# Optimization experiments

Hardware: AMD Instinct MI355X
Metric: run time of the kernel (lower is better)

The kernel has to match this reference:

```python
import jax, jax.numpy as jnp
import numpy as np

D = 512
H = 8
HD = D // H
EPS = 1e-5
NEG_INF = -1e30


def _ln(x, g, b):
    mu = jnp.mean(x, axis=-1, keepdims=True)
    var = jnp.mean(jnp.square(x - mu), axis=-1, keepdims=True)
    return (x - mu) * jax.lax.rsqrt(var + EPS) * g + b


def setup_inputs() -> dict:
    key = jax.random.key(0)
    ks = jax.random.split(key, 8)
    V, M, S = 128, 128, 514  # seq includes 2 head tokens (cls+dist)
    inp = {
        "video_embeds": jax.random.normal(ks[0], (V, D), jnp.float32),
        "music_features": jax.random.normal(ks[1], (M, S, D), jnp.float32),
        "music_masks": jnp.ones((M, S - 2), jnp.int32),
    }
    wk = jax.random.split(ks[2], 5)
    for name, k in zip(["Wq", "Wk", "Wv", "Wo", "Wl"], wk):
        inp[name] = jax.random.normal(k, (D, D), jnp.float32) * 0.02
    for name in ["bq", "bk", "bv", "bo", "bl"]:
        inp[name] = jnp.zeros((D,), jnp.float32)
    for name in ["g1", "g2", "g3"]:
        inp[name] = jnp.ones((D,), jnp.float32)
    for name in ["b1", "b2", "b3"]:
        inp[name] = jnp.zeros((D,), jnp.float32)
    return inp


def reference(video_embeds, music_features, music_masks,
              Wq, bq, Wk, bk, Wv, bv, Wo, bo, Wl, bl,
              g1, b1, g2, b2, g3, b3):
    # drop cls + dist tokens
    mf = music_features[:, 2:, :]  # (M, f, D)
    ve = _ln(video_embeds, g1, b1)  # (V, D)
    mf = _ln(mf, g1, b1)
    V = ve.shape[0]
    M, f, _ = mf.shape

    q = (ve @ Wq.T + bq).reshape(V, H, HD).transpose(1, 0, 2)        # (H, V, hd)
    k = (mf @ Wk.T + bk).reshape(M, f, H, HD).transpose(0, 2, 1, 3)  # (M, H, f, hd)
    v = (mf @ Wv.T + bv).reshape(M, f, H, HD).transpose(0, 2, 1, 3)  # (M, H, f, hd)

    logits = jnp.einsum('hvd,mhfd->vmhf', q, k) / np.sqrt(HD).astype(np.float32)
    mask = music_masks[None, :, None, :]  # (1, M, 1, f)
    logits = jnp.where(mask == 0, NEG_INF, logits)
    w = jax.nn.softmax(logits, axis=-1)
    attn = jnp.einsum('vmhf,mhfd->vmhd', w, v).reshape(V, M, D)
    attn = attn @ Wo.T + bo

    attn = _ln(attn, g2, b2)
    out = attn + (attn @ Wl.T + bl)  # dropout = identity in eval
    return _ln(out, g3, b3)
```

## Files before the change

kernel.cpp:

```cpp
#include <hip/hip_runtime.h>
#include <hip/hip_bf16.h>

typedef unsigned int uint;
typedef unsigned short ushort;
typedef __bf16 bf16;
typedef bf16 bf16x8 __attribute__((ext_vector_type(8)));
typedef float f32x4 __attribute__((ext_vector_type(4)));
typedef ushort ushort4v __attribute__((ext_vector_type(4)));

__device__ __forceinline__ float bf2f(ushort u) {
  union { uint u; float f; } v; v.u = ((uint)u) << 16; return v.f;
}
__device__ __forceinline__ ushort f2bf(float f) {
  union { float f; uint u; } v; v.f = f;
  uint u = v.u;
  uint r = (u + 0x7fffu + ((u >> 16) & 1u)) >> 16;
  return (ushort)r;
}

__device__ __forceinline__ void gl2lds16(const void* g, void* l) {
  __builtin_amdgcn_global_load_lds(
      (const __attribute__((address_space(1))) void*)g,
      (__attribute__((address_space(3))) void*)l, 16, 0, 0);
}

struct CastArgs {
  const float* s0; const float* s1; const float* s2; const float* s3; const float* s4;
  ushort* d0; ushort* d1; ushort* d2; ushort* d3; ushort* d4;
};
__global__ __launch_bounds__(256) void bfcast5(CastArgs a) {
  int t = blockIdx.x * 256 + threadIdx.x;
  int which = t >> 15;
  int e = (t & 32767) * 8;
  const float* s = which == 0 ? a.s0 : which == 1 ? a.s1 : which == 2 ? a.s2 : which == 3 ? a.s3 : a.s4;
  ushort*      d = which == 0 ? a.d0 : which == 1 ? a.d1 : which == 2 ? a.d2 : which == 3 ? a.d3 : a.d4;
  float4 v0 = *(const float4*)(s + e);
  float4 v1 = *(const float4*)(s + e + 4);
  uint4 o;
  o.x = (uint)f2bf(v0.x) | ((uint)f2bf(v0.y) << 16);
  o.y = (uint)f2bf(v0.z) | ((uint)f2bf(v0.w) << 16);
  o.z = (uint)f2bf(v1.x) | ((uint)f2bf(v1.y) << 16);
  o.w = (uint)f2bf(v1.z) | ((uint)f2bf(v1.w) << 16);
  *(uint4*)(d + e) = o;
}

__global__ __launch_bounds__(256) void ln512v(
    int mode, int nrows,
    const void* __restrict__ srcA, const void* __restrict__ srcB,
    const float* __restrict__ g, const float* __restrict__ b,
    void* __restrict__ dst)
{
  const int l = threadIdx.x & 63;
  const int nw = gridDim.x * 4;
  for (int row = blockIdx.x * 4 + (threadIdx.x >> 6); row < nrows; row += nw) {
    float x[8];
    if (mode <= 1) {
      const float* s;
      if (mode == 0) {
        s = (const float*)srcA + (size_t)row * 512;
      } else {
        int mm = row >> 9, fi = row & 511;
        s = (const float*)srcA + ((size_t)mm * 514 + 2 + fi) * 512;
      }
      float4 a0 = *(const float4*)(s + l * 4);
      float4 a1 = *(const float4*)(s + 256 + l * 4);
      x[0] = a0.x; x[1] = a0.y; x[2] = a0.z; x[3] = a0.w;
      x[4] = a1.x; x[5] = a1.y; x[6] = a1.z; x[7] = a1.w;
    } else if (mode == 2) {
      const ushort* s = (const ushort*)srcA + (size_t)row * 512;
      uint4 u = *(const uint4*)(s + l * 8);
      x[0] = bf2f((ushort)u.x); x[1] = bf2f((ushort)(u.x >> 16));
      x[2] = bf2f((ushort)u.y); x[3] = bf2f((ushort)(u.y >> 16));
      x[4] = bf2f((ushort)u.z); x[5] = bf2f((ushort)(u.z >> 16));
      x[6] = bf2f((ushort)u.w); x[7] = bf2f((ushort)(u.w >> 16));
    } else {
      const ushort* sa = (const ushort*)srcA + (size_t)row * 512;
      const ushort* sb = (const ushort*)srcB + (size_t)row * 512;
      uint4 ua = *(const uint4*)(sa + l * 8);
      uint4 ub = *(const uint4*)(sb + l * 8);
      x[0] = bf2f((ushort)ua.x) + bf2f((ushort)ub.x);
      x[1] = bf2f((ushort)(ua.x >> 16)) + bf2f((ushort)(ub.x >> 16));
      x[2] = bf2f((ushort)ua.y) + bf2f((ushort)ub.y);
      x[3] = bf2f((ushort)(ua.y >> 16)) + bf2f((ushort)(ub.y >> 16));
      x[4] = bf2f((ushort)ua.z) + bf2f((ushort)ub.z);
      x[5] = bf2f((ushort)(ua.z >> 16)) + bf2f((ushort)(ub.z >> 16));
      x[6] = bf2f((ushort)ua.w) + bf2f((ushort)ub.w);
      x[7] = bf2f((ushort)(ua.w >> 16)) + bf2f((ushort)(ub.w >> 16));
    }
    float sum = 0.f, sq = 0.f;
    #pragma unroll
    for (int j = 0; j < 8; ++j) { sum += x[j]; sq += x[j] * x[j]; }
    #pragma unroll
    for (int o = 1; o < 64; o <<= 1) {
      sum += __shfl_xor(sum, o);
      sq  += __shfl_xor(sq, o);
    }
    const float inv = 1.f / 512.f;
    float mu = sum * inv;
    float var = sq * inv - mu * mu;
    float rstd = rsqrtf(var + 1e-5f);

    float gv[8], bv[8];
    if (mode <= 1) {
      float4 g0 = *(const float4*)(g + l * 4);
      float4 g1 = *(const float4*)(g + 256 + l * 4);
      float4 b0 = *(const float4*)(b + l * 4);
      float4 b1 = *(const float4*)(b + 256 + l * 4);
      gv[0] = g0.x; gv[1] = g0.y; gv[2] = g0.z; gv[3] = g0.w;
      gv[4] = g1.x; gv[5] = g1.y; gv[6] = g1.z; gv[7] = g1.w;
      bv[0] = b0.x; bv[1] = b0.y; bv[2] = b0.z; bv[3] = b0.w;
      bv[4] = b1.x; bv[5] = b1.y; bv[6] = b1.z; bv[7] = b1.w;
    } else {
      float4 g0 = *(const float4*)(g + l * 8);
      float4 g1 = *(const float4*)(g + l * 8 + 4);
      float4 b0 = *(const float4*)(b + l * 8);
      float4 b1 = *(const float4*)(b + l * 8 + 4);
      gv[0] = g0.x; gv[1] = g0.y; gv[2] = g0.z; gv[3] = g0.w;
      gv[4] = g1.x; gv[5] = g1.y; gv[6] = g1.z; gv[7] = g1.w;
      bv[0] = b0.x; bv[1] = b0.y; bv[2] = b0.z; bv[3] = b0.w;
      bv[4] = b1.x; bv[5] = b1.y; bv[6] = b1.z; bv[7] = b1.w;
    }
    float y[8];
    #pragma unroll
    for (int j = 0; j < 8; ++j) y[j] = (x[j] - mu) * rstd * gv[j] + bv[j];

    if (mode <= 1) {
      ushort* d = (ushort*)dst + (size_t)row * 512;
      ushort4v p0, p1;
      #pragma unroll
      for (int j = 0; j < 4; ++j) { p0[j] = f2bf(y[j]); p1[j] = f2bf(y[4 + j]); }
      *(ushort4v*)(d + l * 4) = p0;
      *(ushort4v*)(d + 256 + l * 4) = p1;
    } else if (mode == 2) {
      ushort* d = (ushort*)dst + (size_t)row * 512;
      uint4 o;
      o.x = (uint)f2bf(y[0]) | ((uint)f2bf(y[1]) << 16);
      o.y = (uint)f2bf(y[2]) | ((uint)f2bf(y[3]) << 16);
      o.z = (uint)f2bf(y[4]) | ((uint)f2bf(y[5]) << 16);
      o.w = (uint)f2bf(y[6]) | ((uint)f2bf(y[7]) << 16);
      *(uint4*)(d + l * 8) = o;
    } else {
      float* d = (float*)dst + (size_t)row * 512;
      float4 o0, o1;
      o0.x = y[0]; o0.y = y[1]; o0.z = y[2]; o0.w = y[3];
      o1.x = y[4]; o1.y = y[5]; o1.z = y[6]; o1.w = y[7];
      *(float4*)(d + l * 8) = o0;
      *(float4*)(d + l * 8 + 4) = o1;
    }
  }
}

__global__ __launch_bounds__(256) void gemm512(
    const ushort* __restrict__ A, const ushort* __restrict__ W,
    const float* __restrict__ bias, ushort* __restrict__ C,
    float scale, int vt_mode)
{
  __shared__ __align__(16) ushort As[128 * 64];
  __shared__ __align__(16) ushort Bs[128 * 64];
  const int tid = threadIdx.x;
  const int w = tid >> 6, l = tid & 63;
  const int lg = l >> 4, lr = l & 15;
  const int wr = w >> 1, wc = w & 1;
  const int row0 = blockIdx.y * 128, col0 = blockIdx.x * 128;

  f32x4 acc[4][4];
  #pragma unroll
  for (int i = 0; i < 4; i++)
    #pragma unroll
    for (int j = 0; j < 4; j++) { f32x4 z = {0.f,0.f,0.f,0.f}; acc[i][j] = z; }

  for (int kk = 0; kk < 8; ++kk) {
    #pragma unroll
    for (int c2 = 0; c2 < 4; ++c2) {
      int c = c2 * 256 + tid;
      int r = c >> 3, j = c & 7;
      int ksrc = kk * 64 + ((j * 8) ^ ((r & 7) * 8));
      gl2lds16(A + (size_t)(row0 + r) * 512 + ksrc, As + (c2 * 256 + w * 64) * 8);
      gl2lds16(W + (size_t)(col0 + r) * 512 + ksrc, Bs + (c2 * 256 + w * 64) * 8);
    }
    __syncthreads();
    #pragma unroll
    for (int k2 = 0; k2 < 2; ++k2) {
      bf16x8 af[4], bfr[4];
      #pragma unroll
      for (int mi = 0; mi < 4; ++mi) {
        int r = wr * 64 + mi * 16 + lr;
        af[mi] = *(const bf16x8*)(As + r * 64 + ((k2 * 32 + lg * 8) ^ ((r & 7) * 8)));
      }
      #pragma unroll
      for (int ni = 0; ni < 4; ++ni) {
        int r = wc * 64 + ni * 16 + lr;
        bfr[ni] = *(const bf16x8*)(Bs + r * 64 + ((k2 * 32 + lg * 8) ^ ((r & 7) * 8)));
      }
      #pragma unroll
      for (int mi = 0; mi < 4; ++mi)
        #pragma unroll
        for (int ni = 0; ni < 4; ++ni)
          acc[mi][ni] = __builtin_amdgcn_mfma_f32_16x16x32_bf16(af[mi], bfr[ni], acc[mi][ni], 0, 0, 0);
    }
    __syncthreads();
  }

  #pragma unroll
  for (int ni = 0; ni < 4; ++ni) {
    int cg = col0 + wc * 64 + ni * 16 + lr;
    float bc = bias[cg];
    #pragma unroll
    for (int mi = 0; mi < 4; ++mi) {
      int rg0 = row0 + wr * 64 + mi * 16 + lg * 4;
      if (!vt_mode) {
        #pragma unroll
        for (int e = 0; e < 4; ++e) {
          float v = (acc[mi][ni][e] + bc) * scale;
          C[(size_t)(rg0 + e) * 512 + cg] = f2bf(v);
        }
      } else {
        int m = rg0 >> 9, fi = rg0 & 511;
        ushort4v pk;
        #pragma unroll
        for (int e = 0; e < 4; ++e) pk[e] = f2bf((acc[mi][ni][e] + bc) * scale);
        *(ushort4v*)(C + (size_t)(m * 512 + cg) * 512 + fi) = pk;
      }
    }
  }
}

__global__ __launch_bounds__(256) void attn_kernel(
    const ushort* __restrict__ q, const ushort* __restrict__ k,
    const ushort* __restrict__ vt, const int* __restrict__ masks,
    ushort* __restrict__ attn)
{
  __shared__ __align__(16) ushort Qs[128 * 64];
  __shared__ __align__(16) ushort Ks[64 * 64];
  __shared__ __align__(16) ushort Vs[64 * 64];
  __shared__ __align__(16) ushort Ps[4][32 * 64];
  __shared__ float maskf[64];
  __shared__ float stats[4][32];

  const int tid = threadIdx.x;
  const int w = tid >> 6, l = tid & 63;
  const int lg = l >> 4, lr = l & 15;
  const int m = blockIdx.x >> 3, h = blockIdx.x & 7;

  const size_t kbase = (size_t)(m * 512) * 512 + h * 64;
  const size_t vbase = (size_t)(m * 512 + h * 64) * 512;

  #pragma unroll
  for (int c2 = 0; c2 < 4; ++c2) {
    int c = c2 * 256 + tid;
    int r = c >> 3, j = c & 7;
    gl2lds16(q + (size_t)r * 512 + h * 64 + ((j * 8) ^ ((r & 7) * 8)),
             Qs + (c2 * 256 + w * 64) * 8);
  }

  f32x4 acc[2][4];
  #pragma unroll
  for (int i = 0; i < 2; i++)
    #pragma unroll
    for (int j = 0; j < 4; j++) { f32x4 z = {0.f,0.f,0.f,0.f}; acc[i][j] = z; }
  float m_run[2] = {-INFINITY, -INFINITY};
  float l_run[2] = {0.f, 0.f};
  bf16x8 qf[2][2];

  for (int it = 0; it < 8; ++it) {
    const int f0 = it * 64;
    #pragma unroll
    for (int c2 = 0; c2 < 2; ++c2) {
      int c = c2 * 256 + tid;
      int r = c >> 3, j = c & 7;
      int off = (j * 8) ^ ((r & 7) * 8);
      gl2lds16(k + kbase + (size_t)(f0 + r) * 512 + off, Ks + (c2 * 256 + w * 64) * 8);
      gl2lds16(vt + vbase + (size_t)r * 512 + f0 + off, Vs + (c2 * 256 + w * 64) * 8);
    }
    if (tid < 64) maskf[tid] = masks[m * 512 + f0 + tid] ? 0.f : -1e30f;
    __syncthreads();

    if (it == 0) {
      #pragma unroll
      for (int nv = 0; nv < 2; ++nv)
        #pragma unroll
        for (int k2 = 0; k2 < 2; ++k2) {
          int v = w * 32 + nv * 16 + lr;
          qf[nv][k2] = *(const bf16x8*)(Qs + v * 64 + ((k2 * 32 + lg * 8) ^ ((v & 7) * 8)));
        }
    }

    f32x4 s[4][2];
    #pragma unroll
    for (int mi = 0; mi < 4; mi++)
      #pragma unroll
      for (int nv = 0; nv < 2; nv++) { f32x4 z = {0.f,0.f,0.f,0.f}; s[mi][nv] = z; }
    #pragma unroll
    for (int k2 = 0; k2 < 2; ++k2) {
      bf16x8 kf[4];
      #pragma unroll
      for (int mi = 0; mi < 4; ++mi) {
        int f = mi * 16 + lr;
        kf[mi] = *(const bf16x8*)(Ks + f * 64 + ((k2 * 32 + lg * 8) ^ ((f & 7) * 8)));
      }
      #pragma unroll
      for (int mi = 0; mi < 4; ++mi)
        #pragma unroll
        for (int nv = 0; nv < 2; ++nv)
          s[mi][nv] = __builtin_amdgcn_mfma_f32_16x16x32_bf16(kf[mi], qf[nv][k2], s[mi][nv], 0, 0, 0);
    }

    float mk[4][4];
    #pragma unroll
    for (int mi = 0; mi < 4; mi++)
      #pragma unroll
      for (int e = 0; e < 4; e++) mk[mi][e] = maskf[mi * 16 + lg * 4 + e];

    #pragma unroll
    for (int nv = 0; nv < 2; ++nv) {
      float cmax = -INFINITY;
      #pragma unroll
      for (int mi = 0; mi < 4; mi++)
        #pragma unroll
        for (int e = 0; e < 4; e++) {
          s[mi][nv][e] += mk[mi][e];
          cmax = fmaxf(cmax, s[mi][nv][e]);
        }
      cmax = fmaxf(cmax, __shfl_xor(cmax, 16));
      cmax = fmaxf(cmax, __shfl_xor(cmax, 32));
      float mnew = fmaxf(m_run[nv], cmax);
      float sc = __expf(m_run[nv] - mnew);
      float csum = 0.f;
      int vloc = nv * 16 + lr;
      #pragma unroll
      for (int mi = 0; mi < 4; mi++) {
        ushort4v pk;
        #pragma unroll
        for (int e = 0; e < 4; e++) {
          float p = __expf(s[mi][nv][e] - mnew);
          csum += p;
          pk[e] = f2bf(p);
        }
        int f = mi * 16 + lg * 4;
        *(ushort4v*)(&Ps[w][vloc * 64 + (f ^ ((vloc & 7) * 8))]) = pk;
      }
      csum += __shfl_xor(csum, 16);
      csum += __shfl_xor(csum, 32);
      l_run[nv] = l_run[nv] * sc + csum;
      m_run[nv] = mnew;
      if (lg == 0) stats[w][vloc] = sc;
    }

    #pragma unroll
    for (int mi2 = 0; mi2 < 2; ++mi2)
      #pragma unroll
      for (int e = 0; e < 4; ++e) {
        float sc = stats[w][mi2 * 16 + lg * 4 + e];
        #pragma unroll
        for (int nd = 0; nd < 4; ++nd) acc[mi2][nd][e] *= sc;
      }

    #pragma unroll
    for (int k2 = 0; k2 < 2; ++k2) {
      bf16x8 pf[2], vf[4];
      #pragma unroll
      for (int mi2 = 0; mi2 < 2; ++mi2) {
        int vloc = mi2 * 16 + lr;
        pf[mi2] = *(const bf16x8*)(&Ps[w][vloc * 64 + ((k2 * 32 + lg * 8) ^ ((vloc & 7) * 8))]);
      }
      #pragma unroll
      for (int nd = 0; nd < 4; ++nd) {
        int d = nd * 16 + lr;
        vf[nd] = *(const bf16x8*)(Vs + d * 64 + ((k2 * 32 + lg * 8) ^ ((d & 7) * 8)));
      }
      #pragma unroll
      for (int mi2 = 0; mi2 < 2; ++mi2)
        #pragma unroll
        for (int nd = 0; nd < 4; ++nd)
          acc[mi2][nd] = __builtin_amdgcn_mfma_f32_16x16x32_bf16(pf[mi2], vf[nd], acc[mi2][nd], 0, 0, 0);
    }
    __syncthreads();
  }

  #pragma unroll
  for (int nv = 0; nv < 2; ++nv)
    if (lg == 0) stats[w][nv * 16 + lr] = 1.f / l_run[nv];
  #pragma unroll
  for (int mi2 = 0; mi2 < 2; ++mi2)
    #pragma unroll
    for (int e = 0; e < 4; ++e) {
      float invl = stats[w][mi2 * 16 + lg * 4 + e];
      int vg = w * 32 + mi2 * 16 + lg * 4 + e;
      #pragma unroll
      for (int nd = 0; nd < 4; ++nd) {
        int d = nd * 16 + lr;
        attn[(size_t)(vg * 128 + m) * 512 + h * 64 + d] = f2bf(acc[mi2][nd][e] * invl);
      }
    }
}

extern "C" void kernel_launch(void* const* d_in, const int* in_sizes, int n_in,
                              void* d_out, int out_size, void* d_ws, size_t ws_size,
                              hipStream_t stream) {
  const float* video = (const float*)d_in[0];
  const float* music = (const float*)d_in[1];
  const int*   masks = (const int*)d_in[2];
  const float* Wq = (const float*)d_in[3];
  const float* Wk = (const float*)d_in[4];
  const float* Wv = (const float*)d_in[5];
  const float* Wo = (const float*)d_in[6];
  const float* Wl = (const float*)d_in[7];
  const float* bq = (const float*)d_in[8];
  const float* bk = (const float*)d_in[9];
  const float* bv = (const float*)d_in[10];
  const float* bo = (const float*)d_in[11];
  const float* bl = (const float*)d_in[12];
  const float* g1 = (const float*)d_in[13];
  const float* g2 = (const float*)d_in[14];
  const float* g3 = (const float*)d_in[15];
  const float* b1 = (const float*)d_in[16];
  const float* b2 = (const float*)d_in[17];
  const float* b3 = (const float*)d_in[18];

  char* ws = (char*)d_ws;
  ushort* mfln = (ushort*)(ws);
  ushort* kbuf = (ushort*)(ws + 67108864);
  ushort* vtb  = (ushort*)(ws + 134217728);
  ushort* attn = (ushort*)(ws + 201326592);
  ushort* c1   = (ushort*)(ws + 218103808);
  ushort* xbuf = (ushort*)(ws + 234881024);
  ushort* veln = (ushort*)(ws + 251658240);
  ushort* qbuf = (ushort*)(ws + 251789312);
  ushort* wqb  = (ushort*)(ws + 251920384);
  ushort* wkb  = wqb + 262144;
  ushort* wvb  = wkb + 262144;
  ushort* wob  = wvb + 262144;
  ushort* wlb  = wob + 262144;

  CastArgs ca = {Wq, Wk, Wv, Wo, Wl, wqb, wkb, wvb, wob, wlb};
  bfcast5<<<640, 256, 0, stream>>>(ca);

  ln512v<<<32, 256, 0, stream>>>(0, 128, video, nullptr, g1, b1, veln);
  ln512v<<<2048, 256, 0, stream>>>(1, 65536, music, nullptr, g1, b1, mfln);

  gemm512<<<dim3(4, 1), 256, 0, stream>>>(veln, wqb, bq, qbuf, 0.125f, 0);
  gemm512<<<dim3(4, 512), 256, 0, stream>>>(mfln, wkb, bk, kbuf, 1.f, 0);
  gemm512<<<dim3(4, 512), 256, 0, stream>>>(mfln, wvb, bv, vtb, 1.f, 1);

  attn_kernel<<<1024, 256, 0, stream>>>(qbuf, kbuf, vtb, masks, attn);

  gemm512<<<dim3(4, 128), 256, 0, stream>>>(attn, wob, bo, c1, 1.f, 0);
  ln512v<<<2048, 256, 0, stream>>>(2, 16384, c1, nullptr, g2, b2, xbuf);
  gemm512<<<dim3(4, 128), 256, 0, stream>>>(xbuf, wlb, bl, c1, 1.f, 0);
  ln512v<<<2048, 256, 0, stream>>>(3, 16384, xbuf, c1, g3, b3, d_out);
}
```

Baseline: 319.9 us.

## Double-buffer GEMM LDS loads, remap tile order, fuse preamble kernels, prioritize MFMA

Merges the weight cast and both input layernorms into one preamble launch to cut launch overhead. The GEMM now double-buffers its LDS tiles so the next k-slice's global-to-LDS loads overlap the current MFMAs, and it remaps block IDs into an XCD-strided order. The attention kernel raises wave priority around its MFMA blocks. LDS use doubles to 64KB per GEMM block, which may reduce occupancy.

```diff
diff --git a/kernel.cpp b/kernel.cpp
--- a/kernel.cpp
+++ b/kernel.cpp
@@ -24,35 +24,15 @@
       (__attribute__((address_space(3))) void*)l, 16, 0, 0);
 }
 
-struct CastArgs {
-  const float* s0; const float* s1; const float* s2; const float* s3; const float* s4;
-  ushort* d0; ushort* d1; ushort* d2; ushort* d3; ushort* d4;
-};
-__global__ __launch_bounds__(256) void bfcast5(CastArgs a) {
-  int t = blockIdx.x * 256 + threadIdx.x;
-  int which = t >> 15;
-  int e = (t & 32767) * 8;
-  const float* s = which == 0 ? a.s0 : which == 1 ? a.s1 : which == 2 ? a.s2 : which == 3 ? a.s3 : a.s4;
-  ushort*      d = which == 0 ? a.d0 : which == 1 ? a.d1 : which == 2 ? a.d2 : which == 3 ? a.d3 : a.d4;
-  float4 v0 = *(const float4*)(s + e);
-  float4 v1 = *(const float4*)(s + e + 4);
-  uint4 o;
-  o.x = (uint)f2bf(v0.x) | ((uint)f2bf(v0.y) << 16);
-  o.y = (uint)f2bf(v0.z) | ((uint)f2bf(v0.w) << 16);
-  o.z = (uint)f2bf(v1.x) | ((uint)f2bf(v1.y) << 16);
-  o.w = (uint)f2bf(v1.z) | ((uint)f2bf(v1.w) << 16);
-  *(uint4*)(d + e) = o;
-}
-
-__global__ __launch_bounds__(256) void ln512v(
-    int mode, int nrows,
+__device__ __forceinline__ void ln_rows(
+    int mode, int nrows, int blk, int nblk, int tid,
     const void* __restrict__ srcA, const void* __restrict__ srcB,
     const float* __restrict__ g, const float* __restrict__ b,
     void* __restrict__ dst)
 {
-  const int l = threadIdx.x & 63;
-  const int nw = gridDim.x * 4;
-  for (int row = blockIdx.x * 4 + (threadIdx.x >> 6); row < nrows; row += nw) {
+  const int l = tid & 63;
+  const int nw = nblk * 4;
+  for (int row = blk * 4 + (tid >> 6); row < nrows; row += nw) {
     float x[8];
     if (mode <= 1) {
       const float* s;
@@ -150,18 +130,62 @@
   }
 }
 
-__global__ __launch_bounds__(256) void gemm512(
+__global__ __launch_bounds__(256) void ln512v(
+    int mode, int nrows,
+    const void* __restrict__ srcA, const void* __restrict__ srcB,
+    const float* __restrict__ g, const float* __restrict__ b,
+    void* __restrict__ dst)
+{
+  ln_rows(mode, nrows, blockIdx.x, gridDim.x, threadIdx.x, srcA, srcB, g, b, dst);
+}
+
+struct PreArgs {
+  const float* s0; const float* s1; const float* s2; const float* s3; const float* s4;
+  ushort* d0; ushort* d1; ushort* d2; ushort* d3; ushort* d4;
+  const float* video; const float* music;
+  const float* g1; const float* b1;
+  ushort* veln; ushort* mfln;
+};
+__global__ __launch_bounds__(256) void preamble(PreArgs a) {
+  int bb = blockIdx.x;
+  if (bb < 640) {
+    int t = bb * 256 + threadIdx.x;
+    int which = t >> 15;
+    int e = (t & 32767) * 8;
+    const float* s = which == 0 ? a.s0 : which == 1 ? a.s1 : which == 2 ? a.s2 : which == 3 ? a.s3 : a.s4;
+    ushort*      d = which == 0 ? a.d0 : which == 1 ? a.d1 : which == 2 ? a.d2 : which == 3 ? a.d3 : a.d4;
+    float4 v0 = *(const float4*)(s + e);
+    float4 v1 = *(const float4*)(s + e + 4);
+    uint4 o;
+    o.x = (uint)f2bf(v0.x) | ((uint)f2bf(v0.y) << 16);
+    o.y = (uint)f2bf(v0.z) | ((uint)f2bf(v0.w) << 16);
+    o.z = (uint)f2bf(v1.x) | ((uint)f2bf(v1.y) << 16);
+    o.w = (uint)f2bf(v1.z) | ((uint)f2bf(v1.w) << 16);
+    *(uint4*)(d + e) = o;
+  } else if (bb < 672) {
+    ln_rows(0, 128, bb - 640, 32, threadIdx.x, a.video, nullptr, a.g1, a.b1, a.veln);
+  } else {
+    ln_rows(1, 65536, bb - 672, 2048, threadIdx.x, a.music, nullptr, a.g1, a.b1, a.mfln);
+  }
+}
+
+__global__ __launch_bounds__(256) void gemm_t3(
     const ushort* __restrict__ A, const ushort* __restrict__ W,
     const float* __restrict__ bias, ushort* __restrict__ C,
     float scale, int vt_mode)
 {
-  __shared__ __align__(16) ushort As[128 * 64];
-  __shared__ __align__(16) ushort Bs[128 * 64];
+  __shared__ __align__(16) ushort As[2][128 * 64];
+  __shared__ __align__(16) ushort Bs[2][128 * 64];
   const int tid = threadIdx.x;
   const int w = tid >> 6, l = tid & 63;
   const int lg = l >> 4, lr = l & 15;
   const int wr = w >> 1, wc = w & 1;
-  const int row0 = blockIdx.y * 128, col0 = blockIdx.x * 128;
+
+  int nwg = gridDim.x * gridDim.y;
+  int bid = blockIdx.y * gridDim.x + blockIdx.x;
+  if ((nwg & 7) == 0) bid = (bid & 7) * (nwg >> 3) + (bid >> 3);
+  const int bx = bid % gridDim.x, by = bid / gridDim.x;
+  const int row0 = by * 128, col0 = bx * 128;
 
   f32x4 acc[4][4];
   #pragma unroll
@@ -169,28 +193,37 @@
     #pragma unroll
     for (int j = 0; j < 4; j++) { f32x4 z = {0.f,0.f,0.f,0.f}; acc[i][j] = z; }
 
-  for (int kk = 0; kk < 8; ++kk) {
+  size_t asrc[4], wsrc[4]; int ldst[4];
+  #pragma unroll
+  for (int c2 = 0; c2 < 4; ++c2) {
+    int c = c2 * 256 + tid;
+    int r = c >> 3, j = c & 7;
+    int koff = (j ^ (r & 7)) * 8;
+    asrc[c2] = (size_t)(row0 + r) * 512 + koff;
+    wsrc[c2] = (size_t)(col0 + r) * 512 + koff;
+    ldst[c2] = (c2 * 256 + w * 64) * 8;
+  }
+
+  auto stage = [&](int pb, int kk) {
     #pragma unroll
     for (int c2 = 0; c2 < 4; ++c2) {
-      int c = c2 * 256 + tid;
-      int r = c >> 3, j = c & 7;
-      int ksrc = kk * 64 + ((j * 8) ^ ((r & 7) * 8));
-      gl2lds16(A + (size_t)(row0 + r) * 512 + ksrc, As + (c2 * 256 + w * 64) * 8);
-      gl2lds16(W + (size_t)(col0 + r) * 512 + ksrc, Bs + (c2 * 256 + w * 64) * 8);
-    }
-    __syncthreads();
-    #pragma unroll
-    for (int k2 = 0; k2 < 2; ++k2) {
+      gl2lds16(A + asrc[c2] + kk * 64, &As[pb][ldst[c2]]);
+      gl2lds16(W + wsrc[c2] + kk * 64, &Bs[pb][ldst[c2]]);
+    }
+  };
+  auto compute = [&](int pb) {
+    #pragma unroll
+    for (int ks = 0; ks < 2; ++ks) {
       bf16x8 af[4], bfr[4];
       #pragma unroll
       for (int mi = 0; mi < 4; ++mi) {
         int r = wr * 64 + mi * 16 + lr;
-        af[mi] = *(const bf16x8*)(As + r * 64 + ((k2 * 32 + lg * 8) ^ ((r & 7) * 8)));
+        af[mi] = *(const bf16x8*)(&As[pb][r * 64 + ((ks * 32 + lg * 8) ^ ((r & 7) * 8))]);
       }
       #pragma unroll
       for (int ni = 0; ni < 4; ++ni) {
         int r = wc * 64 + ni * 16 + lr;
-        bfr[ni] = *(const bf16x8*)(Bs + r * 64 + ((k2 * 32 + lg * 8) ^ ((r & 7) * 8)));
+        bfr[ni] = *(const bf16x8*)(&Bs[pb][r * 64 + ((ks * 32 + lg * 8) ^ ((r & 7) * 8))]);
       }
       #pragma unroll
       for (int mi = 0; mi < 4; ++mi)
@@ -198,8 +231,19 @@
         for (int ni = 0; ni < 4; ++ni)
           acc[mi][ni] = __builtin_amdgcn_mfma_f32_16x16x32_bf16(af[mi], bfr[ni], acc[mi][ni], 0, 0, 0);
     }
+  };
+
+  stage(0, 0);
+  __syncthreads();
+  int cur = 0;
+  #pragma unroll
+  for (int kk = 0; kk < 7; ++kk) {
+    stage(cur ^ 1, kk + 1);
+    compute(cur);
     __syncthreads();
-  }
+    cur ^= 1;
+  }
+  compute(cur);
 
   #pragma unroll
   for (int ni = 0; ni < 4; ++ni) {
@@ -298,11 +342,13 @@
         int f = mi * 16 + lr;
         kf[mi] = *(const bf16x8*)(Ks + f * 64 + ((k2 * 32 + lg * 8) ^ ((f & 7) * 8)));
       }
+      __builtin_amdgcn_s_setprio(1);
       #pragma unroll
       for (int mi = 0; mi < 4; ++mi)
         #pragma unroll
         for (int nv = 0; nv < 2; ++nv)
           s[mi][nv] = __builtin_amdgcn_mfma_f32_16x16x32_bf16(kf[mi], qf[nv][k2], s[mi][nv], 0, 0, 0);
+      __builtin_amdgcn_s_setprio(0);
     }
 
     float mk[4][4];
@@ -368,11 +414,13 @@
         int d = nd * 16 + lr;
         vf[nd] = *(const bf16x8*)(Vs + d * 64 + ((k2 * 32 + lg * 8) ^ ((d & 7) * 8)));
       }
+      __builtin_amdgcn_s_setprio(1);
       #pragma unroll
       for (int mi2 = 0; mi2 < 2; ++mi2)
         #pragma unroll
         for (int nd = 0; nd < 4; ++nd)
           acc[mi2][nd] = __builtin_amdgcn_mfma_f32_16x16x32_bf16(pf[mi2], vf[nd], acc[mi2][nd], 0, 0, 0);
+      __builtin_amdgcn_s_setprio(0);
     }
     __syncthreads();
   }
@@ -432,20 +480,18 @@
   ushort* wob  = wvb + 262144;
   ushort* wlb  = wob + 262144;
 
-  CastArgs ca = {Wq, Wk, Wv, Wo, Wl, wqb, wkb, wvb, wob, wlb};
-  bfcast5<<<640, 256, 0, stream>>>(ca);
-
-  ln512v<<<32, 256, 0, stream>>>(0, 128, video, nullptr, g1, b1, veln);
-  ln512v<<<2048, 256, 0, stream>>>(1, 65536, music, nullptr, g1, b1, mfln);
-
-  gemm512<<<dim3(4, 1), 256, 0, stream>>>(veln, wqb, bq, qbuf, 0.125f, 0);
-  gemm512<<<dim3(4, 512), 256, 0, stream>>>(mfln, wkb, bk, kbuf, 1.f, 0);
-  gemm512<<<dim3(4, 512), 256, 0, stream>>>(mfln, wvb, bv, vtb, 1.f, 1);
+  PreArgs pa = {Wq, Wk, Wv, Wo, Wl, wqb, wkb, wvb, wob, wlb,
+                video, music, g1, b1, veln, mfln};
+  preamble<<<2720, 256, 0, stream>>>(pa);
+
+  gemm_t3<<<dim3(4, 1), 256, 0, stream>>>(veln, wqb, bq, qbuf, 0.125f, 0);
+  gemm_t3<<<dim3(4, 512), 256, 0, stream>>>(mfln, wkb, bk, kbuf, 1.f, 0);
+  gemm_t3<<<dim3(4, 512), 256, 0, stream>>>(mfln, wvb, bv, vtb, 1.f, 1);
 
   attn_kernel<<<1024, 256, 0, stream>>>(qbuf, kbuf, vtb, masks, attn);
 
-  gemm512<<<dim3(4, 128), 256, 0, stream>>>(attn, wob, bo, c1, 1.f, 0);
+  gemm_t3<<<dim3(4, 128), 256, 0, stream>>>(attn, wob, bo, c1, 1.f, 0);
   ln512v<<<2048, 256, 0, stream>>>(2, 16384, c1, nullptr, g2, b2, xbuf);
-  gemm512<<<dim3(4, 128), 256, 0, stream>>>(xbuf, wlb, bl, c1, 1.f, 0);
+  gemm_t3<<<dim3(4, 128), 256, 0, stream>>>(xbuf, wlb, bl, c1, 1.f, 0);
   ln512v<<<2048, 256, 0, stream>>>(3, 16384, xbuf, c1, g3, b3, d_out);
 }
```

Result: faster. 282.3 us (-11.8%).
